# Kernel tuning notes

Measured on AMD Instinct MI355X. Metric: run time of the kernel, lower is better.

Reference implementation:

```python
import jax, jax.numpy as jnp
import numpy as np

WINDOW_SIZE = 11
SIGMA = 1.5
DATA_RANGE = 1.0
C1 = (0.01 * DATA_RANGE) ** 2
C2 = (0.03 * DATA_RANGE) ** 2


def _gaussian_window(size: int, sigma: float) -> jnp.ndarray:
    coords = jnp.arange(size, dtype=jnp.float32) - size // 2
    g = jnp.exp(-(coords ** 2) / (2.0 * sigma ** 2))
    g = g / g.sum()
    w2d = g[:, None] * g[None, :]
    return w2d[None, None, :, :]  # (O=1, I=1, K, K)


def _conv_same(x, window):
    pad = WINDOW_SIZE // 2
    return jax.lax.conv_general_dilated(
        x, window,
        window_strides=(1, 1),
        padding=((pad, pad), (pad, pad)),
        dimension_numbers=("NCHW", "OIHW", "NCHW"),
    )


def setup_inputs() -> dict:
    key = jax.random.key(0)
    kx, ky = jax.random.split(key)
    B, C, H, W = 64, 1, 512, 512
    x = jax.random.uniform(kx, (B, C, H, W), dtype=jnp.float32)
    y = jax.random.uniform(ky, (B, C, H, W), dtype=jnp.float32)
    return {"x": x, "y": y}


def reference(x, y):
    window = _gaussian_window(WINDOW_SIZE, SIGMA)
    mu_x = _conv_same(x, window)
    mu_y = _conv_same(y, window)
    mu_x_sq = mu_x * mu_x
    mu_y_sq = mu_y * mu_y
    mu_xy = mu_x * mu_y
    sigma_x_sq = _conv_same(x * x, window) - mu_x_sq
    sigma_y_sq = _conv_same(y * y, window) - mu_y_sq
    sigma_xy = _conv_same(x * y, window) - mu_xy
    num = (2.0 * mu_xy + C1) * (2.0 * sigma_xy + C2)
    den = (mu_x_sq + mu_y_sq + C1) * (sigma_x_sq + sigma_y_sq + C2)
    ssim_map = num / den
    ssim_val = ssim_map.mean(axis=(1, 2, 3))  # (B,)
    loss = 1.0 - ssim_val
    return loss.mean()  # reduction='mean'
```

## Files before the change

### kernel.cpp

```cpp
#include <hip/hip_runtime.h>
#include <hip/hip_fp16.h>

typedef _Float16 f16x8 __attribute__((ext_vector_type(8)));
typedef float    f32x4 __attribute__((ext_vector_type(4)));
typedef float    f32x2 __attribute__((ext_vector_type(2)));

#define IMG   512
#define NIMG  64
#define TS_C  64
#define NBLK  (NIMG * 8 * 8)
#define XST   80
#define HTS   40
#define SROWS 42

#define C1F   1.0e-4f
#define C2F   9.0e-4f
#define INVSUM 0.26601174f

__device__ __forceinline__ uint2 cvt4h(f32x4 a) {
    __half2 p0 = __floats2half2_rn(a[0], a[1]);
    __half2 p1 = __floats2half2_rn(a[2], a[3]);
    uint2 r; r.x = *reinterpret_cast<uint*>(&p0); r.y = *reinterpret_cast<uint*>(&p1);
    return r;
}

__global__ __launch_bounds__(256, 4)
void ssim_main(const float* __restrict__ x, const float* __restrict__ y,
               float* __restrict__ partial) {
    __shared__ __align__(16) __half XYp[2 * SROWS * XST];
    __shared__ __align__(16) __half Ht[5][TS_C][HTS];
    __shared__ _Float16 wtab[64];
    __shared__ float red[4];

    const int tid  = threadIdx.x;
    const int lane = tid & 63;
    const int wv   = tid >> 6;
    const int l16  = lane & 15;
    const int g16  = lane >> 4;
    const int n0   = wv * 16;

    const int img = blockIdx.z;
    const int by  = blockIdx.y;
    const int c0  = blockIdx.x * TS_C;
    const float* xb = x + (size_t)img * IMG * IMG;
    const float* yb = y + (size_t)img * IMG * IMG;

    if (tid < 64) {
        int d = tid - 18;
        float t = (float)(d - 5);
        float v = __expf(-t * t * (1.0f / 4.5f)) * INVSUM;
        wtab[tid] = ((unsigned)d <= 10u) ? (_Float16)v : (_Float16)0.0f;
    }

    const int row0 = tid / 20;
    const int c40  = tid - row0 * 20;

    auto stage_load = [&](int r0, float4* st) {
        bool interior = (r0 >= 8) & (r0 <= IMG - 37) & (c0 >= 8) & (c0 <= IMG - 72);
        int row_u = row0, c4 = c40;
        #pragma unroll
        for (int i = 0; i < 7; ++i) {
            int  ru = row_u > 83 ? 83 : row_u;
            bool ya = ru >= SROWS;
            int  rp = ya ? ru - SROWS : ru;
            int  gr = r0 - 5 + rp;
            int  gc = c0 - 8 + c4 * 4;
            const float* src = (ya ? yb : xb) + (size_t)gr * IMG + gc;
            if (interior) {
                st[i] = *(const float4*)src;
            } else {
                bool valid = (i < 6) | (tid < 144);
                bool ok = valid & ((unsigned)gr < (unsigned)IMG) & ((unsigned)gc < (unsigned)IMG);
                st[i] = ok ? *(const float4*)src : make_float4(0.f, 0.f, 0.f, 0.f);
            }
            c4 += 16; int inc = 12;
            if (c4 >= 20) { c4 -= 20; inc = 13; }
            row_u += inc;
        }
    };

    auto stage_write = [&](const float4* st) {
        int row_u = row0, c4 = c40;
        #pragma unroll
        for (int i = 0; i < 7; ++i) {
            if (i < 6 || tid < 144) {
                __half2 p0 = __floats2half2_rn(st[i].x, st[i].y);
                __half2 p1 = __floats2half2_rn(st[i].z, st[i].w);
                uint2 v; v.x = *reinterpret_cast<uint*>(&p0); v.y = *reinterpret_cast<uint*>(&p1);
                *(uint2*)&XYp[row_u * XST + c4 * 4] = v;
            }
            c4 += 16; int inc = 12;
            if (c4 >= 20) { c4 -= 20; inc = 13; }
            row_u += inc;
        }
    };

    const int hcol = n0 + l16;
    f32x2 ssum2 = {0.0f, 0.0f};
    f16x8 WhB, WvA;

    auto hpass = [&](int g, int sb) {
        int srow = g * 16 + l16;
        if (srow > SROWS - 1) srow = SROWS - 1;
        int off = srow * XST + n0 + g16 * 8;
        f16x8 xf = *(const f16x8*)&XYp[off];
        f16x8 yf = *(const f16x8*)&XYp[SROWS * XST + off];
        f16x8 xx = xf * xf;
        f16x8 yy = yf * yf;
        f16x8 xy = xf * yf;
        f32x4 z = {0.f, 0.f, 0.f, 0.f};
        f32x4 aX  = __builtin_amdgcn_mfma_f32_16x16x32_f16(xf, WhB, z, 0, 0, 0);
        f32x4 aY  = __builtin_amdgcn_mfma_f32_16x16x32_f16(yf, WhB, z, 0, 0, 0);
        f32x4 aXX = __builtin_amdgcn_mfma_f32_16x16x32_f16(xx, WhB, z, 0, 0, 0);
        f32x4 aYY = __builtin_amdgcn_mfma_f32_16x16x32_f16(yy, WhB, z, 0, 0, 0);
        f32x4 aXY = __builtin_amdgcn_mfma_f32_16x16x32_f16(xy, WhB, z, 0, 0, 0);
        int hrow = sb + g16 * 4;
        *(uint2*)&Ht[0][hcol][hrow] = cvt4h(aX);
        *(uint2*)&Ht[1][hcol][hrow] = cvt4h(aY);
        *(uint2*)&Ht[2][hcol][hrow] = cvt4h(aXX);
        *(uint2*)&Ht[3][hcol][hrow] = cvt4h(aYY);
        *(uint2*)&Ht[4][hcol][hrow] = cvt4h(aXY);
    };

    auto vpass = [&](int mt) {
        int ko = (mt * 16 + g16 * 8) & 31;
        f16x8 b0 = *(const f16x8*)&Ht[0][hcol][ko];
        f16x8 b1 = *(const f16x8*)&Ht[1][hcol][ko];
        f16x8 b2 = *(const f16x8*)&Ht[2][hcol][ko];
        f16x8 b3 = *(const f16x8*)&Ht[3][hcol][ko];
        f16x8 b4 = *(const f16x8*)&Ht[4][hcol][ko];
        f32x4 z = {0.f, 0.f, 0.f, 0.f};
        f32x4 cX  = __builtin_amdgcn_mfma_f32_16x16x32_f16(WvA, b0, z, 0, 0, 0);
        f32x4 cY  = __builtin_amdgcn_mfma_f32_16x16x32_f16(WvA, b1, z, 0, 0, 0);
        f32x4 cXX = __builtin_amdgcn_mfma_f32_16x16x32_f16(WvA, b2, z, 0, 0, 0);
        f32x4 cYY = __builtin_amdgcn_mfma_f32_16x16x32_f16(WvA, b3, z, 0, 0, 0);
        f32x4 cXY = __builtin_amdgcn_mfma_f32_16x16x32_f16(WvA, b4, z, 0, 0, 0);
        #pragma unroll
        for (int h = 0; h < 2; ++h) {
            f32x2 mx  = {cX [2*h], cX [2*h+1]};
            f32x2 my  = {cY [2*h], cY [2*h+1]};
            f32x2 exx = {cXX[2*h], cXX[2*h+1]};
            f32x2 eyy = {cYY[2*h], cYY[2*h+1]};
            f32x2 exy = {cXY[2*h], cXY[2*h+1]};
            f32x2 mxx = mx * mx, myy = my * my, mxy = mx * my;
            f32x2 vx  = exx - mxx;
            f32x2 vy  = eyy - myy;
            f32x2 vxy = exy - mxy;
            f32x2 num = (2.0f * mxy + C1F) * (2.0f * vxy + C2F);
            f32x2 den = (mxx + myy + C1F) * (vx + vy + C2F);
            f32x2 r;
            r[0] = __builtin_amdgcn_rcpf(den[0]);
            r[1] = __builtin_amdgcn_rcpf(den[1]);
            ssum2 += num * r;
        }
    };

    const int r0a = by * 64;
    const int r0b = by * 64 + 32;
    float4 st0[7], st1[7];

    stage_load(r0a, st0);
    stage_write(st0);
    __syncthreads();

    stage_load(r0b, st1);

    {
        const int idx0 = g16 * 8 - l16 + 15;
        _Float16 bv[11];
        #pragma unroll
        for (int j = 0; j < 11; ++j) bv[j] = wtab[idx0 + j];
        #pragma unroll
        for (int j = 0; j < 8; ++j) WhB[j] = bv[j];
        #pragma unroll
        for (int j = 0; j < 8; ++j) WvA[j] = bv[j + 3];
    }

    hpass(0, 0); hpass(1, 16); vpass(0); hpass(2, 0); vpass(1);
    __syncthreads();
    stage_write(st1);
    __syncthreads();
    hpass(0, 0); hpass(1, 16); vpass(0); hpass(2, 0); vpass(1);

    float ssum = ssum2[0] + ssum2[1];
    #pragma unroll
    for (int off = 32; off > 0; off >>= 1)
        ssum += __shfl_down(ssum, off, 64);
    if ((tid & 63) == 0) red[tid >> 6] = ssum;
    __syncthreads();
    if (tid == 0) {
        float tot = red[0] + red[1] + red[2] + red[3];
        int bi = (img * gridDim.y + by) * gridDim.x + blockIdx.x;
        partial[bi] = tot;
    }
}

__global__ __launch_bounds__(1024)
void ssim_final(const float* __restrict__ partial, float* __restrict__ out) {
    __shared__ float red[16];
    float s = 0.0f;
    for (int i = threadIdx.x; i < NBLK; i += 1024) s += partial[i];
    #pragma unroll
    for (int off = 32; off > 0; off >>= 1)
        s += __shfl_down(s, off, 64);
    if ((threadIdx.x & 63) == 0) red[threadIdx.x >> 6] = s;
    __syncthreads();
    if (threadIdx.x == 0) {
        float tot = 0.0f;
        #pragma unroll
        for (int i = 0; i < 16; ++i) tot += red[i];
        out[0] = 1.0f - tot * (1.0f / 16777216.0f);
    }
}

extern "C" void kernel_launch(void* const* d_in, const int* in_sizes, int n_in,
                              void* d_out, int out_size, void* d_ws, size_t ws_size,
                              hipStream_t stream) {
    const float* x = (const float*)d_in[0];
    const float* y = (const float*)d_in[1];
    float* out     = (float*)d_out;
    float* partial = (float*)d_ws;

    dim3 grid(IMG / TS_C, 8, NIMG);
    ssim_main<<<grid, 256, 0, stream>>>(x, y, partial);
    ssim_final<<<1, 1024, 0, stream>>>(partial, out);
}
```

Measured before the change: 48.50 us.

## Stage fp32 tiles via direct global-to-LDS loads, convert to fp16 at read

```diff
diff --git a/kernel.cpp b/kernel.cpp
--- a/kernel.cpp
+++ b/kernel.cpp
@@ -2,19 +2,21 @@
 #include <hip/hip_fp16.h>
 
 typedef _Float16 f16x8 __attribute__((ext_vector_type(8)));
+typedef _Float16 f16x2 __attribute__((ext_vector_type(2)));
 typedef float    f32x4 __attribute__((ext_vector_type(4)));
 typedef float    f32x2 __attribute__((ext_vector_type(2)));
 
-#define IMG   512
-#define NIMG  64
-#define TS_C  64
-#define NBLK  (NIMG * 8 * 8)
-#define XST   80
-#define HTS   40
-#define SROWS 42
-
-#define C1F   1.0e-4f
-#define C2F   9.0e-4f
+#define IMG    512
+#define NIMG   64
+#define TS_C   64
+#define NBLK   (NIMG * 8 * 8)
+#define XSTD   84
+#define PLANE  (42 * XSTD)
+#define UNITS  1764
+#define HTS    36
+
+#define C1F    1.0e-4f
+#define C2F    9.0e-4f
 #define INVSUM 0.26601174f
 
 __device__ __forceinline__ uint2 cvt4h(f32x4 a) {
@@ -24,10 +26,15 @@
     return r;
 }
 
-__global__ __launch_bounds__(256, 4)
+__device__ __forceinline__ f16x2 pkrtz(float a, float b) {
+    auto t = __builtin_amdgcn_cvt_pkrtz(a, b);
+    return __builtin_bit_cast(f16x2, t);
+}
+
+__global__ __launch_bounds__(256, 3)
 void ssim_main(const float* __restrict__ x, const float* __restrict__ y,
                float* __restrict__ partial) {
-    __shared__ __align__(16) __half XYp[2 * SROWS * XST];
+    __shared__ __align__(16) float  XYpF[1792 * 4];
     __shared__ __align__(16) __half Ht[5][TS_C][HTS];
     __shared__ _Float16 wtab[64];
     __shared__ float red[4];
@@ -45,6 +52,8 @@
     const float* xb = x + (size_t)img * IMG * IMG;
     const float* yb = y + (size_t)img * IMG * IMG;
 
+    const bool interior = (blockIdx.x >= 1) & (blockIdx.x <= 6) & (by >= 1) & (by <= 6);
+
     if (tid < 64) {
         int d = tid - 18;
         float t = (float)(d - 5);
@@ -52,46 +61,35 @@
         wtab[tid] = ((unsigned)d <= 10u) ? (_Float16)v : (_Float16)0.0f;
     }
 
-    const int row0 = tid / 20;
-    const int c40  = tid - row0 * 20;
-
-    auto stage_load = [&](int r0, float4* st) {
-        bool interior = (r0 >= 8) & (r0 <= IMG - 37) & (c0 >= 8) & (c0 <= IMG - 72);
+    const int row0 = tid / 21;
+    const int c40  = tid - row0 * 21;
+
+    auto zfill = [&]() {
+        #pragma unroll
+        for (int i = 0; i < 7; ++i)
+            *(f32x4*)&XYpF[(i * 256 + tid) * 4] = (f32x4){0.f, 0.f, 0.f, 0.f};
+    };
+
+    auto stage = [&](int r0t) {
         int row_u = row0, c4 = c40;
         #pragma unroll
         for (int i = 0; i < 7; ++i) {
-            int  ru = row_u > 83 ? 83 : row_u;
-            bool ya = ru >= SROWS;
-            int  rp = ya ? ru - SROWS : ru;
-            int  gr = r0 - 5 + rp;
+            bool ya = row_u >= 42;
+            int  rp = ya ? row_u - 42 : row_u;
+            int  gr = r0t - 5 + rp;
             int  gc = c0 - 8 + c4 * 4;
             const float* src = (ya ? yb : xb) + (size_t)gr * IMG + gc;
-            if (interior) {
-                st[i] = *(const float4*)src;
-            } else {
-                bool valid = (i < 6) | (tid < 144);
-                bool ok = valid & ((unsigned)gr < (unsigned)IMG) & ((unsigned)gc < (unsigned)IMG);
-                st[i] = ok ? *(const float4*)src : make_float4(0.f, 0.f, 0.f, 0.f);
-            }
-            c4 += 16; int inc = 12;
-            if (c4 >= 20) { c4 -= 20; inc = 13; }
-            row_u += inc;
-        }
-    };
-
-    auto stage_write = [&](const float4* st) {
-        int row_u = row0, c4 = c40;
-        #pragma unroll
-        for (int i = 0; i < 7; ++i) {
-            if (i < 6 || tid < 144) {
-                __half2 p0 = __floats2half2_rn(st[i].x, st[i].y);
-                __half2 p1 = __floats2half2_rn(st[i].z, st[i].w);
-                uint2 v; v.x = *reinterpret_cast<uint*>(&p0); v.y = *reinterpret_cast<uint*>(&p1);
-                *(uint2*)&XYp[row_u * XST + c4 * 4] = v;
-            }
-            c4 += 16; int inc = 12;
-            if (c4 >= 20) { c4 -= 20; inc = 13; }
-            row_u += inc;
+            float* dst = &XYpF[(i * 256 + wv * 64) * 4];
+            bool tailok = (i < 6) | (tid < UNITS - 6 * 256);
+            bool ok = interior ? tailok
+                    : (tailok & ((unsigned)gr < (unsigned)IMG)
+                              & ((unsigned)gc <= (unsigned)(IMG - 4)));
+            if (ok)
+                __builtin_amdgcn_global_load_lds(
+                    (const __attribute__((address_space(1))) void*)src,
+                    (__attribute__((address_space(3))) void*)dst, 16, 0, 0);
+            c4 += 4; row_u += 12;
+            if (c4 >= 21) { c4 -= 21; row_u += 1; }
         }
     };
 
@@ -99,12 +97,22 @@
     f32x2 ssum2 = {0.0f, 0.0f};
     f16x8 WhB, WvA;
 
+    union UH { f16x8 v; f16x2 p[4]; };
+
     auto hpass = [&](int g, int sb) {
         int srow = g * 16 + l16;
-        if (srow > SROWS - 1) srow = SROWS - 1;
-        int off = srow * XST + n0 + g16 * 8;
-        f16x8 xf = *(const f16x8*)&XYp[off];
-        f16x8 yf = *(const f16x8*)&XYp[SROWS * XST + off];
+        if (srow > 41) srow = 41;
+        int off = srow * XSTD + n0 + g16 * 8;
+        f32x4 xlo = *(const f32x4*)&XYpF[off];
+        f32x4 xhi = *(const f32x4*)&XYpF[off + 4];
+        f32x4 ylo = *(const f32x4*)&XYpF[PLANE + off];
+        f32x4 yhi = *(const f32x4*)&XYpF[PLANE + off + 4];
+        UH ux, uy;
+        ux.p[0] = pkrtz(xlo[0], xlo[1]); ux.p[1] = pkrtz(xlo[2], xlo[3]);
+        ux.p[2] = pkrtz(xhi[0], xhi[1]); ux.p[3] = pkrtz(xhi[2], xhi[3]);
+        uy.p[0] = pkrtz(ylo[0], ylo[1]); uy.p[1] = pkrtz(ylo[2], ylo[3]);
+        uy.p[2] = pkrtz(yhi[0], yhi[1]); uy.p[3] = pkrtz(yhi[2], yhi[3]);
+        f16x8 xf = ux.v, yf = uy.v;
         f16x8 xx = xf * xf;
         f16x8 yy = yf * yf;
         f16x8 xy = xf * yf;
@@ -155,15 +163,16 @@
         }
     };
 
+    auto compute = [&]() {
+        hpass(0, 0); hpass(1, 16); vpass(0); hpass(2, 0); vpass(1);
+    };
+
     const int r0a = by * 64;
     const int r0b = by * 64 + 32;
-    float4 st0[7], st1[7];
-
-    stage_load(r0a, st0);
-    stage_write(st0);
-    __syncthreads();
-
-    stage_load(r0b, st1);
+
+    if (!interior) { zfill(); __syncthreads(); }
+    stage(r0a);
+    __syncthreads();
 
     {
         const int idx0 = g16 * 8 - l16 + 15;
@@ -176,11 +185,12 @@
         for (int j = 0; j < 8; ++j) WvA[j] = bv[j + 3];
     }
 
-    hpass(0, 0); hpass(1, 16); vpass(0); hpass(2, 0); vpass(1);
-    __syncthreads();
-    stage_write(st1);
-    __syncthreads();
-    hpass(0, 0); hpass(1, 16); vpass(0); hpass(2, 0); vpass(1);
+    compute();
+    __syncthreads();
+    if (!interior) { zfill(); __syncthreads(); }
+    stage(r0b);
+    __syncthreads();
+    compute();
 
     float ssum = ssum2[0] + ssum2[1];
     #pragma unroll
```

After: 49.34 us. About the same (+1.7%).
